# Kernel optimization log

Hardware: AMD Instinct MI355X
Metric: run time of the kernel (lower is better)

Reference implementation:

```python
import jax, jax.numpy as jnp
import numpy as np
from jax import lax

BOS, EOS = 62, 63
NEG_BIG = -10000.0


def setup_inputs() -> dict:
    key = jax.random.key(0)
    k_em, k_tag, k_len, k_tr = jax.random.split(key, 4)
    B, S, L = 512, 1024, 64
    emissions = jax.random.normal(k_em, (B, S, L), dtype=jnp.float32)
    tags = jax.random.randint(k_tag, (B, S), 0, 62).astype(jnp.int64)
    # valid-prefix mask from random lengths in [S//2, S]
    lengths = jax.random.randint(k_len, (B,), S // 2, S + 1)
    mask = (jnp.arange(S)[None, :] < lengths[:, None]).astype(jnp.float32)
    # transitions: uniform(-0.1, 0.1) with BOS/EOS constraints as in init_weights
    transitions = jax.random.uniform(k_tr, (L, L), minval=-0.1, maxval=0.1, dtype=jnp.float32)
    transitions = transitions.at[:, BOS].set(NEG_BIG)
    transitions = transitions.at[EOS, :].set(NEG_BIG)
    return {"emissions": emissions, "tags": tags, "mask": mask, "transitions": transitions}


def _crf_nll(emissions, tags, mask, transitions):
    B, S, L = emissions.shape
    # ----- gold-path scores -----
    first_tags = tags[:, 0]
    last_idx = (mask.sum(axis=1).astype(jnp.int32) - 1)  # (B,)
    last_tags = jnp.take_along_axis(tags, last_idx[:, None].astype(tags.dtype), axis=1)[:, 0]
    scores = transitions[BOS, first_tags]
    scores = scores + jnp.take_along_axis(emissions[:, 0], first_tags[:, None], axis=1)[:, 0]
    prev_t, cur_t = tags[:, :-1], tags[:, 1:]
    e_step = jnp.take_along_axis(emissions[:, 1:], cur_t[..., None], axis=-1)[..., 0]  # (B,S-1)
    t_step = transitions[prev_t, cur_t]  # (B,S-1)
    scores = scores + jnp.sum((e_step + t_step) * mask[:, 1:], axis=1)
    scores = scores + transitions[last_tags, EOS]
    # ----- log-partition via forward algorithm -----
    alpha0 = transitions[BOS][None, :] + emissions[:, 0]  # (B,L)
    em_t = jnp.moveaxis(emissions[:, 1:], 1, 0)  # (S-1,B,L)
    mk_t = mask[:, 1:].T  # (S-1,B)

    def step(alpha, xs):
        e_t, m_t = xs
        # alpha[b,i] + T[i,j] + e_t[b,j] -> logsumexp over i
        new = jax.nn.logsumexp(alpha[:, :, None] + transitions[None, :, :] + e_t[:, None, :], axis=1)
        return jnp.where(m_t[:, None] > 0, new, alpha), None

    alpha, _ = lax.scan(step, alpha0, (em_t, mk_t))
    partition = jax.nn.logsumexp(alpha + transitions[:, EOS][None, :], axis=1)  # (B,)
    return -jnp.sum(scores - partition)


def reference(emissions, tags, mask, transitions):
    return _crf_nll(emissions, tags, mask, transitions)
```

## Files before the change

kernel.cpp:

```cpp
#include <hip/hip_runtime.h>
#include <math.h>

#define BOS_TAG 62
#define EOS_TAG 63
#define S_LEN   1024
#define NCH     32
#define CH      32
#define WPB     2
#define LN2F    0.69314718055994530942f

typedef short  short8 __attribute__((ext_vector_type(8)));
typedef unsigned short ushort4v __attribute__((ext_vector_type(4)));
typedef float  f32x4  __attribute__((ext_vector_type(4)));

template <int CTRL>
__device__ __forceinline__ int dpp_mov(int v) {
  return __builtin_amdgcn_update_dpp(v, v, CTRL, 0xf, 0xf, false);
}
template <int CTRL>
__device__ __forceinline__ float dpp_fmax_step(float v) {
  return fmaxf(v, __int_as_float(dpp_mov<CTRL>(__float_as_int(v))));
}
__device__ __forceinline__ float wave_fmax_all(float v) {
  v = dpp_fmax_step<0x111>(v); v = dpp_fmax_step<0x112>(v);
  v = dpp_fmax_step<0x114>(v); v = dpp_fmax_step<0x118>(v);
  v = dpp_fmax_step<0x142>(v); v = dpp_fmax_step<0x143>(v);
  return __int_as_float(__builtin_amdgcn_readlane(__float_as_int(v), 63));
}
template <int CTRL>
__device__ __forceinline__ float dpp_fadd_step(float v) {
  int t = __builtin_amdgcn_update_dpp(0, __float_as_int(v), CTRL, 0xf, 0xf, true);
  return v + __int_as_float(t);
}
__device__ __forceinline__ float wave_sum_all(float v) {
  v = dpp_fadd_step<0x111>(v); v = dpp_fadd_step<0x112>(v);
  v = dpp_fadd_step<0x114>(v); v = dpp_fadd_step<0x118>(v);
  v = dpp_fadd_step<0x142>(v); v = dpp_fadd_step<0x143>(v);
  return __int_as_float(__builtin_amdgcn_readlane(__float_as_int(v), 63));
}
__device__ __forceinline__ unsigned short f2bf(float v) {
  return (unsigned short)((__float_as_uint(v) + 0x8000u) >> 16);
}
__device__ __forceinline__ float bf2f(unsigned short u) {
  return __uint_as_float(((unsigned)u) << 16);
}

__global__ __launch_bounds__(256) void crf_lens(
    const float* __restrict__ mask, int* __restrict__ lens, int B)
{
  const int b = blockIdx.x * 4 + (threadIdx.x >> 6);
  if (b >= B) return;
  const int l = threadIdx.x & 63;
  const float4* mb = (const float4*)(mask + (size_t)b * S_LEN);
  float s = 0.f;
#pragma unroll
  for (int i = 0; i < 4; ++i) { float4 q = mb[l + 64 * i]; s += q.x + q.y + q.z + q.w; }
  s = wave_sum_all(s);
  if (l == 0) lens[b] = max(1, min(S_LEN, (int)(s + 0.5f)));
}

__global__ __launch_bounds__(256) void crf_ptab(
    const float* __restrict__ trans, short8* __restrict__ pfrag,
    float* __restrict__ tvf)
{
  const int tid = threadIdx.x;
  for (int e = tid; e < 1024; e += 256) {
    int lane = e & 63, n = (e >> 6) & 3, kc = (e >> 8) & 1, dir = e >> 9;
    int g = lane >> 4, c = lane & 15, col = 4 * c + n;
    short8 f;
#pragma unroll
    for (int j = 0; j < 8; ++j) {
      int k = kc * 32 + g * 8 + j;
      float tv = dir ? trans[col * 64 + k] : trans[k * 64 + col];
      f[j] = (short)f2bf(__expf(tv));
    }
    pfrag[e] = f;
  }
  if (tid < 64) tvf[tid] = __expf(trans[tid * 64 + EOS_TAG]);
}

__global__ __launch_bounds__(256, 3) void crf_chunk_mfma(
    const float* __restrict__ em, const float* __restrict__ trans,
    const int* __restrict__ lens, const short8* __restrict__ pfrag,
    unsigned short* __restrict__ Vf, unsigned short* __restrict__ Vb,
    float* __restrict__ sf, float* __restrict__ sb,
    float* __restrict__ m0a, int B)
{
  __shared__ unsigned short smem[4][16 * 64];
  const int wv = threadIdx.x >> 6;
  const int l  = threadIdx.x & 63;
  const int w  = blockIdx.x * 4 + wv;
  const int nwaves = 2 * B * WPB;
  if (w >= nwaves) return;
  const int dir  = w & 1;
  const int idx  = w >> 1;
  const int b    = idx / WPB;
  const int half = idx % WPB;
  unsigned short* smw = smem[wv];
  const float* embase = em + (size_t)b * S_LEN * 64;
  const int g = l >> 4, c = l & 15;

  const int len = lens[b];

  float v_row0 = 1.0f;
  if (dir == 0 && half == 0) {
    float a0 = trans[BOS_TAG * 64 + l] + embase[l];
    float m0 = wave_fmax_all(a0);
    v_row0 = __expf(a0 - m0);
    if (l == 0) m0a[b] = m0;
  }

  unsigned short* Vout = dir ? Vb : Vf;
  float* sout = dir ? sb : sf;
  int fstep[16];
  int ps = -1, pr = -1;
#pragma unroll
  for (int r = 0; r < 16; ++r) {
    int kg = half * 16 + r;
    int tend = min((kg + 1) * CH, len - 1);
    fstep[r] = tend - (kg * CH + 1);
    if (fstep[r] < 0) {
      Vout[((size_t)b * NCH + kg) * 64 + l] = 0x3F80;
      if (l == 0) sout[b * NCH + kg] = 0.f;
    }
    if (fstep[r] >= 0 && fstep[r] < CH - 1) { ps = fstep[r]; pr = r; }
  }

  if (half * 16 * CH + 1 > len - 1) return;

  short8 Bf[2][4];
  {
    const short8* pf = pfrag + dir * 512;
#pragma unroll
    for (int kc = 0; kc < 2; ++kc)
#pragma unroll
      for (int n = 0; n < 4; ++n)
        Bf[kc][n] = pf[(kc * 4 + n) * 64 + l];
  }

#pragma unroll
  for (int r = 0; r < 16; ++r) {
    float v = (dir == 0 && half == 0 && r == 0) ? v_row0 : 1.0f;
    smw[(r * 64 + l) ^ ((r & 7) << 3)] = f2bf(v);
  }

  const int byteA0 = (c * 128 + g * 16) ^ ((c & 7) << 4);
  const int byteA1 = (c * 128 + 64 + g * 16) ^ ((c & 7) << 4);
  int sigma = 0;

  auto renorm16 = [&](float* d) {
    float m = d[0];
#pragma unroll
    for (int i = 1; i < 16; ++i) m = fmaxf(m, d[i]);
    m = wave_fmax_all(m);
    int e = ((__float_as_int(m) >> 23) & 0xff) - 127;
    float s = __int_as_float((127 - e) << 23);
#pragma unroll
    for (int i = 0; i < 16; ++i) d[i] *= s;
    sigma += e;
  };
  auto save_row = [&](int r) {
    unsigned short v = smw[(r * 64 + l) ^ ((r & 7) << 3)];
    int kg = half * 16 + r;
    Vout[((size_t)b * NCH + kg) * 64 + l] = v;
    if (l == 0) sout[b * NCH + kg] = (float)sigma;
  };
  auto write_d = [&](const float* d) {
#pragma unroll
    for (int reg = 0; reg < 4; ++reg) {
      int row = g * 4 + reg;
      ushort4v wq;
#pragma unroll
      for (int n = 0; n < 4; ++n) wq[n] = f2bf(d[reg * 4 + n]);
      *reinterpret_cast<ushort4v*>(
          (char*)smw + ((row * 128 + c * 8) ^ ((row & 7) << 4))) = wq;
    }
  };

  if (dir == 0) {
    int tb0[4];
#pragma unroll
    for (int reg = 0; reg < 4; ++reg) tb0[reg] = (half * 16 + g * 4 + reg) * CH + 1;

    auto loadF = [&](float4* q, int tl) {
#pragma unroll
      for (int reg = 0; reg < 4; ++reg) {
        int tr = min(tb0[reg] + tl, S_LEN - 1);
        q[reg] = *reinterpret_cast<const float4*>(embase + (size_t)tr * 64 + 4 * c);
      }
    };
    auto bodyF = [&](const float4* q, int tl, bool rn) {
      f32x4 acc[4];
      {
        short8 a0 = *reinterpret_cast<const short8*>((const char*)smw + byteA0);
        short8 a1 = *reinterpret_cast<const short8*>((const char*)smw + byteA1);
#pragma unroll
        for (int n = 0; n < 4; ++n) {
          f32x4 z = {0.f, 0.f, 0.f, 0.f};
          z = __builtin_amdgcn_mfma_f32_16x16x32_bf16(a0, Bf[0][n], z, 0, 0, 0);
          acc[n] = __builtin_amdgcn_mfma_f32_16x16x32_bf16(a1, Bf[1][n], z, 0, 0, 0);
        }
      }
      float d[16];
#pragma unroll
      for (int reg = 0; reg < 4; ++reg) {
        d[reg * 4 + 0] = acc[0][reg] * __expf(q[reg].x);
        d[reg * 4 + 1] = acc[1][reg] * __expf(q[reg].y);
        d[reg * 4 + 2] = acc[2][reg] * __expf(q[reg].z);
        d[reg * 4 + 3] = acc[3][reg] * __expf(q[reg].w);
      }
      if (rn) renorm16(d);
      write_d(d);
      if (tl == ps) save_row(pr);
    };

    float4 p0[4], p1[4], p2[4], p3[4];
    loadF(p0, 0); loadF(p1, 1); loadF(p2, 2); loadF(p3, 3);
#pragma unroll 1
    for (int t4 = 0; t4 < CH; t4 += 4) {
      bodyF(p0, t4 + 0, false); loadF(p0, t4 + 4);
      bodyF(p1, t4 + 1, false); loadF(p1, t4 + 5);
      bodyF(p2, t4 + 2, false); loadF(p2, t4 + 6);
      bodyF(p3, t4 + 3, true);  loadF(p3, t4 + 7);
    }
#pragma unroll
    for (int r = 0; r < 16; ++r)
      if (fstep[r] == CH - 1) save_row(r);
  } else {
    const int tendl = min((half * 16 + c + 1) * CH, len - 1);

    auto loadB = [&](float4* q, int tl) {
      int tr = max(tendl - tl, 0);
      const float* rowp = embase + (size_t)tr * 64;
      q[0] = *reinterpret_cast<const float4*>(rowp + 8 * g);
      q[1] = *reinterpret_cast<const float4*>(rowp + 8 * g + 4);
      q[2] = *reinterpret_cast<const float4*>(rowp + 32 + 8 * g);
      q[3] = *reinterpret_cast<const float4*>(rowp + 32 + 8 * g + 4);
    };
    auto bodyB = [&](const float4* q, int tl, bool rn) {
      short8 ar0 = *reinterpret_cast<const short8*>((const char*)smw + byteA0);
      short8 ar1 = *reinterpret_cast<const short8*>((const char*)smw + byteA1);
      short8 a0, a1;
#pragma unroll
      for (int j = 0; j < 4; ++j) {
        a0[j]     = (short)f2bf(bf2f((unsigned short)ar0[j])     * __expf(((const float*)&q[0])[j]));
        a0[4 + j] = (short)f2bf(bf2f((unsigned short)ar0[4 + j]) * __expf(((const float*)&q[1])[j]));
        a1[j]     = (short)f2bf(bf2f((unsigned short)ar1[j])     * __expf(((const float*)&q[2])[j]));
        a1[4 + j] = (short)f2bf(bf2f((unsigned short)ar1[4 + j]) * __expf(((const float*)&q[3])[j]));
      }
      f32x4 acc[4];
#pragma unroll
      for (int n = 0; n < 4; ++n) {
        f32x4 z = {0.f, 0.f, 0.f, 0.f};
        z = __builtin_amdgcn_mfma_f32_16x16x32_bf16(a0, Bf[0][n], z, 0, 0, 0);
        acc[n] = __builtin_amdgcn_mfma_f32_16x16x32_bf16(a1, Bf[1][n], z, 0, 0, 0);
      }
      float d[16];
#pragma unroll
      for (int reg = 0; reg < 4; ++reg)
#pragma unroll
        for (int n = 0; n < 4; ++n) d[reg * 4 + n] = acc[n][reg];
      if (rn) renorm16(d);
      write_d(d);
      if (tl == ps) save_row(pr);
    };

    float4 p0[4], p1[4], p2[4], p3[4];
    loadB(p0, 0); loadB(p1, 1); loadB(p2, 2); loadB(p3, 3);
#pragma unroll 1
    for (int t4 = 0; t4 < CH; t4 += 4) {
      bodyB(p0, t4 + 0, false); loadB(p0, t4 + 4);
      bodyB(p1, t4 + 1, false); loadB(p1, t4 + 5);
      bodyB(p2, t4 + 2, false); loadB(p2, t4 + 6);
      bodyB(p3, t4 + 3, true);  loadB(p3, t4 + 7);
    }
#pragma unroll
    for (int r = 0; r < 16; ++r)
      if (fstep[r] == CH - 1) save_row(r);
  }
}

__global__ __launch_bounds__(256) void crf_combine(
    const float* __restrict__ em, const int* __restrict__ tags,
    const float* __restrict__ trans, const int* __restrict__ lens,
    const unsigned short* __restrict__ Vf, const unsigned short* __restrict__ Vb,
    const float* __restrict__ sf, const float* __restrict__ sb,
    const float* __restrict__ m0a, const float* __restrict__ tvf,
    float* __restrict__ term, int B)
{
  const int item = blockIdx.x * 4 + (threadIdx.x >> 6);
  if (item >= B * NCH) return;
  const int b = item / NCH, k = item - b * NCH;
  const int l = threadIdx.x & 63;
  const int len = lens[b];
  const int kb = (len >= 2) ? (len - 2) / CH : 0;

  const int* tb = tags + (size_t)b * S_LEN;
  const float* emb = em + (size_t)b * S_LEN * 64;

  float t = 0.f;
  {
    float sc = 0.f;
    int t0 = k * CH + 1 + l;
    if (l < CH && t0 <= len - 1) {
      int cur = tb[t0], prev = tb[t0 - 1];
      sc = emb[(size_t)t0 * 64 + cur] + trans[prev * 64 + cur];
    }
    if (k == 0) {
      if (l == 32) sc += trans[BOS_TAG * 64 + tb[0]] + emb[tb[0]];
      if (l == 33) sc += trans[tb[len - 1] * 64 + EOS_TAG];
    }
    t -= wave_sum_all(sc);
  }

  const unsigned short* vf = Vf + ((size_t)b * NCH + k) * 64;
  if (k == 0) {
    float v0 = bf2f(vf[l]);
    if (kb == 0) {
      t += m0a[b] + LN2F * sf[b * NCH] + __logf(wave_sum_all(v0 * tvf[l]));
    } else {
      t += m0a[b] + LN2F * (sf[b * NCH] + sb[b * NCH + 1])
         + __logf(wave_sum_all(v0 * bf2f(Vb[((size_t)b * NCH + 1) * 64 + l])));
    }
  } else if (k < kb) {
    float vk = bf2f(vf[l]);
    t += LN2F * sb[b * NCH + k + 1]
       + __logf(wave_sum_all(vk * bf2f(Vb[((size_t)b * NCH + k + 1) * 64 + l])))
       - __logf(wave_sum_all(vk));
  } else if (k == kb) {
    float vk = bf2f(vf[l]);
    t += __logf(wave_sum_all(vk * tvf[l])) - __logf(wave_sum_all(vk));
  }

  if (l == 0) term[item] = t;
}

__global__ __launch_bounds__(1024) void crf_final(
    const float* __restrict__ term, float* __restrict__ out, int n)
{
  __shared__ float red[16];
  float s = 0.f;
  for (int i = threadIdx.x; i < n; i += 1024) s += term[i];
  s = wave_sum_all(s);
  const int wid = threadIdx.x >> 6;
  if ((threadIdx.x & 63) == 0) red[wid] = s;
  __syncthreads();
  if (threadIdx.x == 0) {
    float tot = 0.f;
#pragma unroll
    for (int i = 0; i < 16; ++i) tot += red[i];
    out[0] = tot;
  }
}

__global__ __launch_bounds__(64) void crf_mono(
    const float* __restrict__ em, const int* __restrict__ tags,
    const float* __restrict__ mask, const float* __restrict__ trans,
    float* __restrict__ partial)
{
  const int b = blockIdx.x;
  const int l = threadIdx.x;
  const float* emb = em + (size_t)b * S_LEN * 64;
  const float* mb = mask + (size_t)b * S_LEN;
  float lenf = 0.f;
  for (int t = l; t < S_LEN; t += 64) lenf += mb[t];
  lenf = wave_sum_all(lenf);
  const int len = max(1, min(S_LEN, (int)(lenf + 0.5f)));

  float p[64];
#pragma unroll
  for (int i = 0; i < 64; ++i) p[i] = __expf(trans[i * 64 + l]) * 0.015625f;

  const int* tb = tags + (size_t)b * S_LEN;
  float sc = 0.f;
  for (int tt = 1 + l; tt <= len - 1; tt += 64)
    sc += emb[(size_t)tt * 64 + tb[tt]] + trans[tb[tt - 1] * 64 + tb[tt]];
  sc = wave_sum_all(sc);
  sc += trans[BOS_TAG * 64 + tb[0]] + emb[tb[0]] + trans[tb[len - 1] * 64 + EOS_TAG];

  float a0 = trans[BOS_TAG * 64 + l] + emb[l];
  float m0 = wave_fmax_all(a0);
  float v = __expf(a0 - m0);
  int sigma = 0;
  for (int t = 1; t <= len - 1; ++t) {
    float E = __expf(emb[(size_t)t * 64 + l]);
    int xi = __float_as_int(v);
    float s0 = 0.f, s1 = 0.f, s2 = 0.f, s3 = 0.f;
#pragma unroll
    for (int i = 0; i < 64; i += 4) {
      s0 = fmaf(__int_as_float(__builtin_amdgcn_readlane(xi, i + 0)), p[i + 0], s0);
      s1 = fmaf(__int_as_float(__builtin_amdgcn_readlane(xi, i + 1)), p[i + 1], s1);
      s2 = fmaf(__int_as_float(__builtin_amdgcn_readlane(xi, i + 2)), p[i + 2], s2);
      s3 = fmaf(__int_as_float(__builtin_amdgcn_readlane(xi, i + 3)), p[i + 3], s3);
    }
    v = ((s0 + s1) + (s2 + s3)) * E;
    float m = wave_fmax_all(v);
    int e = ((__float_as_int(m) >> 23) & 0xff) - 127;
    sigma += e + 6;
    v *= __int_as_float((127 - e) << 23);
  }
  float tvec = __expf(trans[l * 64 + EOS_TAG]);
  float lp = m0 + LN2F * (float)sigma + __logf(wave_sum_all(v * tvec));
  if (l == 0) partial[b] = lp - sc;
}

extern "C" void kernel_launch(void* const* d_in, const int* in_sizes, int n_in,
                              void* d_out, int out_size, void* d_ws, size_t ws_size,
                              hipStream_t stream) {
  const float* em = (const float*)d_in[0];
  const int* tags = (const int*)d_in[1];
  const float* mask = (const float*)d_in[2];
  const float* trans = (const float*)d_in[3];
  float* out = (float*)d_out;

  const int B = in_sizes[1] / S_LEN;

  const size_t nSig = (size_t)B * NCH;
  const size_t nV   = (size_t)B * NCH * 64;
  const size_t need = 16384 + 64 * sizeof(float)
                    + (3 * nSig + (size_t)B) * sizeof(float)
                    + (size_t)B * sizeof(int)
                    + 2 * nV * sizeof(unsigned short);

  if (ws_size >= need) {
    short8* pfrag = (short8*)d_ws;
    float* tvf  = (float*)((char*)d_ws + 16384);
    float* sf   = tvf + 64;
    float* sb   = sf + nSig;
    float* m0a  = sb + nSig;
    float* term = m0a + B;
    int*   lens = (int*)(term + nSig);
    unsigned short* Vf = (unsigned short*)(lens + B);
    unsigned short* Vb = Vf + nV;

    crf_lens<<<(B + 3) / 4, 256, 0, stream>>>(mask, lens, B);
    crf_ptab<<<1, 256, 0, stream>>>(trans, pfrag, tvf);
    const int nwaves = 2 * B * WPB;
    crf_chunk_mfma<<<(nwaves + 3) / 4, 256, 0, stream>>>(
        em, trans, lens, pfrag, Vf, Vb, sf, sb, m0a, B);
    crf_combine<<<(B * NCH + 3) / 4, 256, 0, stream>>>(
        em, tags, trans, lens, Vf, Vb, sf, sb, m0a, tvf, term, B);
    crf_final<<<1, 1024, 0, stream>>>(term, out, B * NCH);
  } else {
    float* partial = (float*)d_ws;
    crf_mono<<<B, 64, 0, stream>>>(em, tags, mask, trans, partial);
    crf_final<<<1, 1024, 0, stream>>>(partial, out, B);
  }
}
```

Before: 73.73 us.

## Interleave forward and backward chunk recurrences within one wave for ILP

Each wave now runs both the forward and backward chunked recurrences, alternating their steps, instead of giving each direction its own wave. The two independent dependency chains can hide each other's MFMA, LDS and exp latency, and the wave count is halved. The costs are roughly double the register use per wave (launch bound lowered to 1), fewer waves to hide memory latency, and a shallower load prefetch of two steps per direction instead of four.

```diff
diff --git a/kernel.cpp b/kernel.cpp
--- a/kernel.cpp
+++ b/kernel.cpp
@@ -79,39 +79,36 @@
   if (tid < 64) tvf[tid] = __expf(trans[tid * 64 + EOS_TAG]);
 }
 
-__global__ __launch_bounds__(256, 3) void crf_chunk_mfma(
+__global__ __launch_bounds__(256, 1) void crf_chunk_mfma(
     const float* __restrict__ em, const float* __restrict__ trans,
     const int* __restrict__ lens, const short8* __restrict__ pfrag,
     unsigned short* __restrict__ Vf, unsigned short* __restrict__ Vb,
     float* __restrict__ sf, float* __restrict__ sb,
     float* __restrict__ m0a, int B)
 {
-  __shared__ unsigned short smem[4][16 * 64];
+  __shared__ unsigned short smem[4][2][16 * 64];
   const int wv = threadIdx.x >> 6;
   const int l  = threadIdx.x & 63;
   const int w  = blockIdx.x * 4 + wv;
-  const int nwaves = 2 * B * WPB;
+  const int nwaves = B * WPB;
   if (w >= nwaves) return;
-  const int dir  = w & 1;
-  const int idx  = w >> 1;
-  const int b    = idx / WPB;
-  const int half = idx % WPB;
-  unsigned short* smw = smem[wv];
+  const int b    = w / WPB;
+  const int half = w % WPB;
+  unsigned short* smf = smem[wv][0];
+  unsigned short* smb = smem[wv][1];
   const float* embase = em + (size_t)b * S_LEN * 64;
   const int g = l >> 4, c = l & 15;
 
   const int len = lens[b];
 
   float v_row0 = 1.0f;
-  if (dir == 0 && half == 0) {
+  if (half == 0) {
     float a0 = trans[BOS_TAG * 64 + l] + embase[l];
     float m0 = wave_fmax_all(a0);
     v_row0 = __expf(a0 - m0);
     if (l == 0) m0a[b] = m0;
   }
 
-  unsigned short* Vout = dir ? Vb : Vf;
-  float* sout = dir ? sb : sf;
   int fstep[16];
   int ps = -1, pr = -1;
 #pragma unroll
@@ -120,35 +117,36 @@
     int tend = min((kg + 1) * CH, len - 1);
     fstep[r] = tend - (kg * CH + 1);
     if (fstep[r] < 0) {
-      Vout[((size_t)b * NCH + kg) * 64 + l] = 0x3F80;
-      if (l == 0) sout[b * NCH + kg] = 0.f;
+      Vf[((size_t)b * NCH + kg) * 64 + l] = 0x3F80;
+      Vb[((size_t)b * NCH + kg) * 64 + l] = 0x3F80;
+      if (l == 0) { sf[b * NCH + kg] = 0.f; sb[b * NCH + kg] = 0.f; }
     }
     if (fstep[r] >= 0 && fstep[r] < CH - 1) { ps = fstep[r]; pr = r; }
   }
 
   if (half * 16 * CH + 1 > len - 1) return;
 
-  short8 Bf[2][4];
-  {
-    const short8* pf = pfrag + dir * 512;
-#pragma unroll
-    for (int kc = 0; kc < 2; ++kc)
-#pragma unroll
-      for (int n = 0; n < 4; ++n)
-        Bf[kc][n] = pf[(kc * 4 + n) * 64 + l];
-  }
+  short8 BfF[2][4], BfB[2][4];
+#pragma unroll
+  for (int kc = 0; kc < 2; ++kc)
+#pragma unroll
+    for (int n = 0; n < 4; ++n) {
+      BfF[kc][n] = pfrag[(kc * 4 + n) * 64 + l];
+      BfB[kc][n] = pfrag[512 + (kc * 4 + n) * 64 + l];
+    }
 
 #pragma unroll
   for (int r = 0; r < 16; ++r) {
-    float v = (dir == 0 && half == 0 && r == 0) ? v_row0 : 1.0f;
-    smw[(r * 64 + l) ^ ((r & 7) << 3)] = f2bf(v);
+    float vf0 = (half == 0 && r == 0) ? v_row0 : 1.0f;
+    smf[(r * 64 + l) ^ ((r & 7) << 3)] = f2bf(vf0);
+    smb[(r * 64 + l) ^ ((r & 7) << 3)] = f2bf(1.0f);
   }
 
   const int byteA0 = (c * 128 + g * 16) ^ ((c & 7) << 4);
   const int byteA1 = (c * 128 + 64 + g * 16) ^ ((c & 7) << 4);
-  int sigma = 0;
-
-  auto renorm16 = [&](float* d) {
+  int sigF = 0, sigB = 0;
+
+  auto renorm16 = [&](float* d, int& sig) {
     float m = d[0];
 #pragma unroll
     for (int i = 1; i < 16; ++i) m = fmaxf(m, d[i]);
@@ -157,15 +155,16 @@
     float s = __int_as_float((127 - e) << 23);
 #pragma unroll
     for (int i = 0; i < 16; ++i) d[i] *= s;
-    sigma += e;
-  };
-  auto save_row = [&](int r) {
+    sig += e;
+  };
+  auto save_row = [&](int r, const unsigned short* smw,
+                      unsigned short* Vout, float* sout, int sig) {
     unsigned short v = smw[(r * 64 + l) ^ ((r & 7) << 3)];
     int kg = half * 16 + r;
     Vout[((size_t)b * NCH + kg) * 64 + l] = v;
-    if (l == 0) sout[b * NCH + kg] = (float)sigma;
-  };
-  auto write_d = [&](const float* d) {
+    if (l == 0) sout[b * NCH + kg] = (float)sig;
+  };
+  auto write_d = [&](const float* d, unsigned short* smw) {
 #pragma unroll
     for (int reg = 0; reg < 4; ++reg) {
       int row = g * 4 + reg;
@@ -177,107 +176,98 @@
     }
   };
 
-  if (dir == 0) {
-    int tb0[4];
-#pragma unroll
-    for (int reg = 0; reg < 4; ++reg) tb0[reg] = (half * 16 + g * 4 + reg) * CH + 1;
-
-    auto loadF = [&](float4* q, int tl) {
-#pragma unroll
-      for (int reg = 0; reg < 4; ++reg) {
-        int tr = min(tb0[reg] + tl, S_LEN - 1);
-        q[reg] = *reinterpret_cast<const float4*>(embase + (size_t)tr * 64 + 4 * c);
-      }
-    };
-    auto bodyF = [&](const float4* q, int tl, bool rn) {
-      f32x4 acc[4];
-      {
-        short8 a0 = *reinterpret_cast<const short8*>((const char*)smw + byteA0);
-        short8 a1 = *reinterpret_cast<const short8*>((const char*)smw + byteA1);
-#pragma unroll
-        for (int n = 0; n < 4; ++n) {
-          f32x4 z = {0.f, 0.f, 0.f, 0.f};
-          z = __builtin_amdgcn_mfma_f32_16x16x32_bf16(a0, Bf[0][n], z, 0, 0, 0);
-          acc[n] = __builtin_amdgcn_mfma_f32_16x16x32_bf16(a1, Bf[1][n], z, 0, 0, 0);
-        }
-      }
-      float d[16];
-#pragma unroll
-      for (int reg = 0; reg < 4; ++reg) {
-        d[reg * 4 + 0] = acc[0][reg] * __expf(q[reg].x);
-        d[reg * 4 + 1] = acc[1][reg] * __expf(q[reg].y);
-        d[reg * 4 + 2] = acc[2][reg] * __expf(q[reg].z);
-        d[reg * 4 + 3] = acc[3][reg] * __expf(q[reg].w);
-      }
-      if (rn) renorm16(d);
-      write_d(d);
-      if (tl == ps) save_row(pr);
-    };
-
-    float4 p0[4], p1[4], p2[4], p3[4];
-    loadF(p0, 0); loadF(p1, 1); loadF(p2, 2); loadF(p3, 3);
-#pragma unroll 1
-    for (int t4 = 0; t4 < CH; t4 += 4) {
-      bodyF(p0, t4 + 0, false); loadF(p0, t4 + 4);
-      bodyF(p1, t4 + 1, false); loadF(p1, t4 + 5);
-      bodyF(p2, t4 + 2, false); loadF(p2, t4 + 6);
-      bodyF(p3, t4 + 3, true);  loadF(p3, t4 + 7);
-    }
-#pragma unroll
-    for (int r = 0; r < 16; ++r)
-      if (fstep[r] == CH - 1) save_row(r);
-  } else {
-    const int tendl = min((half * 16 + c + 1) * CH, len - 1);
-
-    auto loadB = [&](float4* q, int tl) {
-      int tr = max(tendl - tl, 0);
-      const float* rowp = embase + (size_t)tr * 64;
-      q[0] = *reinterpret_cast<const float4*>(rowp + 8 * g);
-      q[1] = *reinterpret_cast<const float4*>(rowp + 8 * g + 4);
-      q[2] = *reinterpret_cast<const float4*>(rowp + 32 + 8 * g);
-      q[3] = *reinterpret_cast<const float4*>(rowp + 32 + 8 * g + 4);
-    };
-    auto bodyB = [&](const float4* q, int tl, bool rn) {
-      short8 ar0 = *reinterpret_cast<const short8*>((const char*)smw + byteA0);
-      short8 ar1 = *reinterpret_cast<const short8*>((const char*)smw + byteA1);
-      short8 a0, a1;
-#pragma unroll
-      for (int j = 0; j < 4; ++j) {
-        a0[j]     = (short)f2bf(bf2f((unsigned short)ar0[j])     * __expf(((const float*)&q[0])[j]));
-        a0[4 + j] = (short)f2bf(bf2f((unsigned short)ar0[4 + j]) * __expf(((const float*)&q[1])[j]));
-        a1[j]     = (short)f2bf(bf2f((unsigned short)ar1[j])     * __expf(((const float*)&q[2])[j]));
-        a1[4 + j] = (short)f2bf(bf2f((unsigned short)ar1[4 + j]) * __expf(((const float*)&q[3])[j]));
-      }
-      f32x4 acc[4];
+  int tb0[4];
+#pragma unroll
+  for (int reg = 0; reg < 4; ++reg) tb0[reg] = (half * 16 + g * 4 + reg) * CH + 1;
+  const int tendl = min((half * 16 + c + 1) * CH, len - 1);
+
+  auto loadF = [&](float4* q, int tl) {
+#pragma unroll
+    for (int reg = 0; reg < 4; ++reg) {
+      int tr = min(tb0[reg] + tl, S_LEN - 1);
+      q[reg] = *reinterpret_cast<const float4*>(embase + (size_t)tr * 64 + 4 * c);
+    }
+  };
+  auto loadB = [&](float4* q, int tl) {
+    int tr = max(tendl - tl, 0);
+    const float* rowp = embase + (size_t)tr * 64;
+    q[0] = *reinterpret_cast<const float4*>(rowp + 8 * g);
+    q[1] = *reinterpret_cast<const float4*>(rowp + 8 * g + 4);
+    q[2] = *reinterpret_cast<const float4*>(rowp + 32 + 8 * g);
+    q[3] = *reinterpret_cast<const float4*>(rowp + 32 + 8 * g + 4);
+  };
+
+  auto bodyF = [&](const float4* q, int tl, bool rn) {
+    f32x4 acc[4];
+    {
+      short8 a0 = *reinterpret_cast<const short8*>((const char*)smf + byteA0);
+      short8 a1 = *reinterpret_cast<const short8*>((const char*)smf + byteA1);
 #pragma unroll
       for (int n = 0; n < 4; ++n) {
         f32x4 z = {0.f, 0.f, 0.f, 0.f};
-        z = __builtin_amdgcn_mfma_f32_16x16x32_bf16(a0, Bf[0][n], z, 0, 0, 0);
-        acc[n] = __builtin_amdgcn_mfma_f32_16x16x32_bf16(a1, Bf[1][n], z, 0, 0, 0);
+        z = __builtin_amdgcn_mfma_f32_16x16x32_bf16(a0, BfF[0][n], z, 0, 0, 0);
+        acc[n] = __builtin_amdgcn_mfma_f32_16x16x32_bf16(a1, BfF[1][n], z, 0, 0, 0);
       }
-      float d[16];
-#pragma unroll
-      for (int reg = 0; reg < 4; ++reg)
-#pragma unroll
-        for (int n = 0; n < 4; ++n) d[reg * 4 + n] = acc[n][reg];
-      if (rn) renorm16(d);
-      write_d(d);
-      if (tl == ps) save_row(pr);
-    };
-
-    float4 p0[4], p1[4], p2[4], p3[4];
-    loadB(p0, 0); loadB(p1, 1); loadB(p2, 2); loadB(p3, 3);
+    }
+    float d[16];
+#pragma unroll
+    for (int reg = 0; reg < 4; ++reg) {
+      d[reg * 4 + 0] = acc[0][reg] * __expf(q[reg].x);
+      d[reg * 4 + 1] = acc[1][reg] * __expf(q[reg].y);
+      d[reg * 4 + 2] = acc[2][reg] * __expf(q[reg].z);
+      d[reg * 4 + 3] = acc[3][reg] * __expf(q[reg].w);
+    }
+    if (rn) renorm16(d, sigF);
+    write_d(d, smf);
+    if (tl == ps) save_row(pr, smf, Vf, sf, sigF);
+  };
+  auto bodyB = [&](const float4* q, int tl, bool rn) {
+    short8 ar0 = *reinterpret_cast<const short8*>((const char*)smb + byteA0);
+    short8 ar1 = *reinterpret_cast<const short8*>((const char*)smb + byteA1);
+    short8 a0, a1;
+#pragma unroll
+    for (int j = 0; j < 4; ++j) {
+      a0[j]     = (short)f2bf(bf2f((unsigned short)ar0[j])     * __expf(((const float*)&q[0])[j]));
+      a0[4 + j] = (short)f2bf(bf2f((unsigned short)ar0[4 + j]) * __expf(((const float*)&q[1])[j]));
+      a1[j]     = (short)f2bf(bf2f((unsigned short)ar1[j])     * __expf(((const float*)&q[2])[j]));
+      a1[4 + j] = (short)f2bf(bf2f((unsigned short)ar1[4 + j]) * __expf(((const float*)&q[3])[j]));
+    }
+    f32x4 acc[4];
+#pragma unroll
+    for (int n = 0; n < 4; ++n) {
+      f32x4 z = {0.f, 0.f, 0.f, 0.f};
+      z = __builtin_amdgcn_mfma_f32_16x16x32_bf16(a0, BfB[0][n], z, 0, 0, 0);
+      acc[n] = __builtin_amdgcn_mfma_f32_16x16x32_bf16(a1, BfB[1][n], z, 0, 0, 0);
+    }
+    float d[16];
+#pragma unroll
+    for (int reg = 0; reg < 4; ++reg)
+#pragma unroll
+      for (int n = 0; n < 4; ++n) d[reg * 4 + n] = acc[n][reg];
+    if (rn) renorm16(d, sigB);
+    write_d(d, smb);
+    if (tl == ps) save_row(pr, smb, Vb, sb, sigB);
+  };
+
+  float4 pf0[4], pf1[4], pb0[4], pb1[4];
+  loadF(pf0, 0); loadB(pb0, 0); loadF(pf1, 1); loadB(pb1, 1);
 #pragma unroll 1
-    for (int t4 = 0; t4 < CH; t4 += 4) {
-      bodyB(p0, t4 + 0, false); loadB(p0, t4 + 4);
-      bodyB(p1, t4 + 1, false); loadB(p1, t4 + 5);
-      bodyB(p2, t4 + 2, false); loadB(p2, t4 + 6);
-      bodyB(p3, t4 + 3, true);  loadB(p3, t4 + 7);
-    }
-#pragma unroll
-    for (int r = 0; r < 16; ++r)
-      if (fstep[r] == CH - 1) save_row(r);
-  }
+  for (int t4 = 0; t4 < CH; t4 += 4) {
+    bodyF(pf0, t4 + 0, false); loadF(pf0, t4 + 2);
+    bodyB(pb0, t4 + 0, false); loadB(pb0, t4 + 2);
+    bodyF(pf1, t4 + 1, false); loadF(pf1, t4 + 3);
+    bodyB(pb1, t4 + 1, false); loadB(pb1, t4 + 3);
+    bodyF(pf0, t4 + 2, false); loadF(pf0, t4 + 4);
+    bodyB(pb0, t4 + 2, false); loadB(pb0, t4 + 4);
+    bodyF(pf1, t4 + 3, true);  loadF(pf1, t4 + 5);
+    bodyB(pb1, t4 + 3, true);  loadB(pb1, t4 + 5);
+  }
+#pragma unroll
+  for (int r = 0; r < 16; ++r)
+    if (fstep[r] == CH - 1) {
+      save_row(r, smf, Vf, sf, sigF);
+      save_row(r, smb, Vb, sb, sigB);
+    }
 }
 
 __global__ __launch_bounds__(256) void crf_combine(
@@ -435,7 +425,7 @@
 
     crf_lens<<<(B + 3) / 4, 256, 0, stream>>>(mask, lens, B);
     crf_ptab<<<1, 256, 0, stream>>>(trans, pfrag, tvf);
-    const int nwaves = 2 * B * WPB;
+    const int nwaves = B * WPB;
     crf_chunk_mfma<<<(nwaves + 3) / 4, 256, 0, stream>>>(
         em, trans, lens, pfrag, Vf, Vb, sf, sb, m0a, B);
     crf_combine<<<(B * NCH + 3) / 4, 256, 0, stream>>>(
```

Result: faster. 70.36 us (-4.6%).
